# Kernel tuning notes

Hardware: AMD Instinct MI355X
Metric: run time of the kernel (lower is better)

The kernel has to match this reference:

```python
import jax, jax.numpy as jnp
import numpy as np

N_NODES = 50000
N_EDGES = 800000
D_IN = 128
HIDDEN = 128
N_CLASSES = 10
N_GRAPHS = 128


def setup_inputs() -> dict:
    key = jax.random.key(0)
    ks = jax.random.split(key, 16)
    x = jax.random.normal(ks[0], (N_NODES, D_IN), dtype=jnp.float32)
    edge_index = jax.random.randint(ks[1], (2, N_EDGES), 0, N_NODES, dtype=jnp.int64)
    batch = jnp.sort(jax.random.randint(ks[2], (N_NODES,), 0, N_GRAPHS, dtype=jnp.int64))

    def lin(k, fin, fout):
        return jax.random.normal(k, (fin, fout), dtype=jnp.float32) / np.sqrt(fin)

    inp = {"x": x, "edge_index": edge_index, "batch": batch}
    # SAGEConv layer 1: in=D_IN, out=HIDDEN; layers 2,3: HIDDEN->HIDDEN
    dims = [(D_IN, HIDDEN), (HIDDEN, HIDDEN), (HIDDEN, HIDDEN)]
    for i, (fin, fout) in enumerate(dims, start=1):
        inp[f"Wl{i}"] = lin(ks[2 + 2 * i], fin, fout)       # neighbor transform
        inp[f"bl{i}"] = jnp.zeros((fout,), dtype=jnp.float32)
        inp[f"Wr{i}"] = lin(ks[3 + 2 * i], fin, fout)       # root transform
    inp["W1"] = lin(ks[12], HIDDEN, HIDDEN)
    inp["b1"] = jnp.zeros((HIDDEN,), dtype=jnp.float32)
    inp["W2"] = lin(ks[13], HIDDEN, N_CLASSES)
    inp["b2"] = jnp.zeros((N_CLASSES,), dtype=jnp.float32)
    return inp


def _sage_conv(x, src, dst, Wl, bl, Wr):
    # mean-aggregate neighbor features then linear; plus root linear (PyG SAGEConv)
    msg = x[src]                                               # [E, d] gather
    agg = jax.ops.segment_sum(msg, dst, num_segments=N_NODES)  # [N, d]
    cnt = jax.ops.segment_sum(jnp.ones_like(dst, dtype=x.dtype), dst,
                              num_segments=N_NODES)
    agg = agg / jnp.maximum(cnt, 1.0)[:, None]
    return agg @ Wl + bl + x @ Wr


def reference(x, edge_index, batch, Wl1, bl1, Wr1, Wl2, bl2, Wr2,
              Wl3, bl3, Wr3, W1, b1, W2, b2):
    src, dst = edge_index[0], edge_index[1]
    h = jax.nn.relu(_sage_conv(x, src, dst, Wl1, bl1, Wr1))
    h = jax.nn.relu(_sage_conv(h, src, dst, Wl2, bl2, Wr2))
    h = jax.nn.relu(_sage_conv(h, src, dst, Wl3, bl3, Wr3))
    # global_mean_pool over graph ids
    gsum = jax.ops.segment_sum(h, batch, num_segments=N_GRAPHS)
    gcnt = jax.ops.segment_sum(jnp.ones((h.shape[0],), h.dtype), batch,
                               num_segments=N_GRAPHS)
    g = gsum / jnp.maximum(gcnt, 1.0)[:, None]                 # [G, hidden]
    g = jax.nn.relu(g @ W1 + b1)
    # dropout is identity at inference (training=False)
    logits = g @ W2 + b2
    return jax.nn.log_softmax(logits, axis=-1)
```

## Files before the change

### kernel.cpp

```cpp
#include <hip/hip_runtime.h>

#define NN 50000
#define NE 800000
#define D 128
#define NG 128
#define POOL_NODES 128
#define SCAN_NB ((NN + 1023) / 1024)
#define NGRP 8
#define GRPSZ 6250
#define FILL_NB 392
#define ESL ((NE + 48) / 49)

typedef __attribute__((ext_vector_type(8))) short bf16x8;
typedef __attribute__((ext_vector_type(4))) float f32x4;

static __device__ __forceinline__ ushort f2bf(float f) {
    uint x = __float_as_uint(f);
    x += 0x7fffu + ((x >> 16) & 1u);
    return (ushort)(x >> 16);
}
static __device__ __forceinline__ float bf2f(ushort u) { return __uint_as_float((uint)u << 16); }
static __device__ __forceinline__ float blo16(uint u) { return __uint_as_float(u << 16); }
static __device__ __forceinline__ float bhi16(uint u) { return __uint_as_float(u & 0xffff0000u); }

#define CASTX_NB 6250
#define CASTW_NB 192
#define COUNT_NB 3125
__global__ __launch_bounds__(256) void fusedA_kernel(
    const float* __restrict__ x, ushort* __restrict__ xb,
    const float* __restrict__ Wl1, const float* __restrict__ Wr1,
    const float* __restrict__ Wl2, const float* __restrict__ Wr2,
    const float* __restrict__ Wl3, const float* __restrict__ Wr3,
    ushort* __restrict__ wlh, ushort* __restrict__ wll,
    ushort* __restrict__ wrh, ushort* __restrict__ wrl,
    const int* __restrict__ dst, int* __restrict__ cnt) {
    const int bid = blockIdx.x;
    if (bid < CASTX_NB) {
        int i = bid * 256 + threadIdx.x;
        int n = i >> 5, g = i & 31;
        float4 v = *reinterpret_cast<const float4*>(x + (size_t)n * D + g * 4);
        ushort4 o;
        o.x = f2bf(v.x); o.y = f2bf(v.y); o.z = f2bf(v.z); o.w = f2bf(v.w);
        *reinterpret_cast<ushort4*>(xb + (size_t)n * D + g * 4) = o;
    } else if (bid < CASTX_NB + CASTW_NB) {
        int i = (bid - CASTX_NB) * 256 + threadIdx.x;
        int layer = i >> 14, j = i & 16383;
        int colg = j >> 7, k = j & 127;
        const float* Wl = (layer == 0) ? Wl1 : ((layer == 1) ? Wl2 : Wl3);
        const float* Wr = (layer == 0) ? Wr1 : ((layer == 1) ? Wr2 : Wr3);
        float vl = Wl[k * 128 + colg];
        float vr = Wr[k * 128 + colg];
        ushort hl = f2bf(vl), hr = f2bf(vr);
        wlh[i] = hl; wll[i] = f2bf(vl - bf2f(hl));
        wrh[i] = hr; wrl[i] = f2bf(vr - bf2f(hr));
    } else {
        int e = (bid - CASTX_NB - CASTW_NB) * 256 + threadIdx.x;
        if (e < NE) atomicAdd(&cnt[dst[e]], 1);
    }
}

__global__ __launch_bounds__(256) void blocksum_kernel(const int* __restrict__ cnt,
                                                       int* __restrict__ bsum, int N) {
    int base = blockIdx.x * 1024 + threadIdx.x * 4;
    int s = 0;
    if (base + 3 < N) {
        int4 v = *reinterpret_cast<const int4*>(cnt + base);
        s = v.x + v.y + v.z + v.w;
    } else {
        for (int i = 0; i < 4; ++i) if (base + i < N) s += cnt[base + i];
    }
    for (int off = 32; off > 0; off >>= 1) s += __shfl_down(s, off, 64);
    __shared__ int wsum[4];
    if ((threadIdx.x & 63) == 0) wsum[threadIdx.x >> 6] = s;
    __syncthreads();
    if (threadIdx.x == 0) bsum[blockIdx.x] = wsum[0] + wsum[1] + wsum[2] + wsum[3];
}

__global__ void scansum_kernel(int* __restrict__ bsum, int* __restrict__ rowptr, int NB, int N) {
    int t = threadIdx.x;
    int v = (t < NB) ? bsum[t] : 0;
    for (int off = 1; off < 64; off <<= 1) {
        int u = __shfl_up(v, off, 64);
        if (t >= off) v += u;
    }
    if (t < NB) bsum[t] = v;
    if (t == NB - 1) rowptr[N] = v;
}

__global__ __launch_bounds__(256) void writeptr_kernel(const int* __restrict__ cnt,
                                                       const int* __restrict__ bsum,
                                                       int* __restrict__ rowptr, int N) {
    const int b = blockIdx.x;
    const int base = b * 1024 + threadIdx.x * 4;
    int vals[4];
#pragma unroll
    for (int i = 0; i < 4; ++i) vals[i] = (base + i < N) ? cnt[base + i] : 0;
    int s = vals[0] + vals[1] + vals[2] + vals[3];

    const int lane = threadIdx.x & 63, w = threadIdx.x >> 6;
    int incl = s;
    for (int off = 1; off < 64; off <<= 1) {
        int u = __shfl_up(incl, off, 64);
        if (lane >= off) incl += u;
    }
    __shared__ int wsum[4];
    if (lane == 63) wsum[w] = incl;
    __syncthreads();
    int excl = (b == 0) ? 0 : bsum[b - 1];
    for (int i = 0; i < w; ++i) excl += wsum[i];
    excl += incl - s;

    int run = excl;
#pragma unroll
    for (int i = 0; i < 4; ++i) {
        if (base + i < N) { rowptr[base + i] = run; run += vals[i]; }
    }
}

static __device__ __forceinline__ void gemm2_body(
    char* As, int rb,
    const ushort* __restrict__ ain,
    const ushort* __restrict__ wlh, const ushort* __restrict__ wll,
    const ushort* __restrict__ wrh, const ushort* __restrict__ wrl,
    const float* __restrict__ bl,
    ushort* __restrict__ y, ushort* __restrict__ z, int N) {
    const int tid = threadIdx.x;
    const int w = tid >> 6, lane = tid & 63;
    const int row0 = rb * 128;
    const int lrow = lane & 15, lk = lane >> 4;
    const int colg = w * 16 + lrow;

    bf16x8 ylh[4], yll[4], zrh[4], zrl[4];
#pragma unroll
    for (int kb = 0; kb < 4; ++kb) {
        int off = colg * 128 + kb * 32 + lk * 8;
        ylh[kb] = *reinterpret_cast<const bf16x8*>(wlh + off);
        yll[kb] = *reinterpret_cast<const bf16x8*>(wll + off);
        zrh[kb] = *reinterpret_cast<const bf16x8*>(wrh + off);
        zrl[kb] = *reinterpret_cast<const bf16x8*>(wrl + off);
    }
    const float bias = bl[colg];

    {
        const char* gbase = (const char*)ain + (size_t)row0 * 256;
#pragma unroll
        for (int i = 0; i < 4; ++i) {
            int Ld = i * 8192 + w * 1024 + lane * 16;
            int gs = Ld ^ (((Ld >> 8) & 7) << 4);
            __builtin_amdgcn_global_load_lds(
                (const uint*)(gbase + gs),
                (uint*)(As + i * 8192 + w * 1024), 16, 0, 0);
        }
    }
    __syncthreads();

#pragma unroll
    for (int mt = 0; mt < 8; ++mt) {
        const int ar = mt * 16 + lrow;
        const int swz = (ar & 7) << 4;
        const char* ap = As + ar * 256;
        bf16x8 ah[4];
#pragma unroll
        for (int kb = 0; kb < 4; ++kb) {
            int b_ = kb * 64 + lk * 16;
            ah[kb] = *reinterpret_cast<const bf16x8*>(ap + (b_ ^ swz));
        }
        f32x4 accy = {0.f, 0.f, 0.f, 0.f}, accz = {0.f, 0.f, 0.f, 0.f};
#pragma unroll
        for (int kb = 0; kb < 4; ++kb) {
            accy = __builtin_amdgcn_mfma_f32_16x16x32_bf16(ah[kb], ylh[kb], accy, 0, 0, 0);
            accy = __builtin_amdgcn_mfma_f32_16x16x32_bf16(ah[kb], yll[kb], accy, 0, 0, 0);
            accz = __builtin_amdgcn_mfma_f32_16x16x32_bf16(ah[kb], zrh[kb], accz, 0, 0, 0);
            accz = __builtin_amdgcn_mfma_f32_16x16x32_bf16(ah[kb], zrl[kb], accz, 0, 0, 0);
        }
#pragma unroll
        for (int r = 0; r < 4; ++r) {
            int rowg = row0 + mt * 16 + lk * 4 + r;
            if (rowg < N) {
                y[(size_t)rowg * D + colg] = f2bf(accy[r]);
                z[(size_t)rowg * D + colg] = f2bf(accz[r] + bias);
            }
        }
    }
}

__global__ __launch_bounds__(512, 4) void gemm2_kernel(
    const ushort* __restrict__ ain,
    const ushort* __restrict__ wlh, const ushort* __restrict__ wll,
    const ushort* __restrict__ wrh, const ushort* __restrict__ wrl,
    const float* __restrict__ bl,
    ushort* __restrict__ y, ushort* __restrict__ z, int N) {
    __shared__ char As[128 * 256];
    gemm2_body(As, blockIdx.x, ain, wlh, wll, wrh, wrl, bl, y, z, N);
}

#define GEMM_NB 391
__global__ __launch_bounds__(512, 4) void fusedB_kernel(
    const ushort* __restrict__ ain,
    const ushort* __restrict__ wlh, const ushort* __restrict__ wll,
    const ushort* __restrict__ wrh, const ushort* __restrict__ wrl,
    const float* __restrict__ bl,
    ushort* __restrict__ y, ushort* __restrict__ z,
    const int* __restrict__ src, const int* __restrict__ dst,
    const int* __restrict__ rowptr, int* __restrict__ fillp,
    int* __restrict__ col, int N) {
    __shared__ char As[128 * 256];
    const int bid = blockIdx.x;
    if (bid < FILL_NB) {
        const int grp = bid & 7;
        const int slice = bid >> 3;
        const int dlo = grp * GRPSZ, dhi = dlo + GRPSZ;
        const int e0 = slice * ESL;
        const int e1 = min(e0 + ESL, NE);
        for (int e = e0 + (int)threadIdx.x; e < e1; e += 512) {
            int d = dst[e];
            if (d >= dlo && d < dhi) {
                int s = src[e];
                int pos = atomicAdd(&fillp[d], 1);
                col[rowptr[d] + pos] = s;
            }
        }
    } else {
        gemm2_body(As, bid - FILL_NB, ain, wlh, wll, wrh, wrl, bl, y, z, N);
    }
}

__global__ __launch_bounds__(256) void gather_relu(
    const ushort* __restrict__ y, ushort* __restrict__ z,
    const int* __restrict__ rowptr, const int* __restrict__ col, int N) {
    int wid = (blockIdx.x * 256 + threadIdx.x) >> 6;
    if (wid >= N) return;
    const int lane = threadIdx.x & 63;
    const int h = lane >> 5, li = lane & 31;
    int lo = rowptr[wid], hi = rowptr[wid + 1];
    float a0 = 0.f, a1 = 0.f, a2 = 0.f, a3 = 0.f;
    int e = lo + h;
    for (; e + 2 < hi; e += 4) {
        int s0 = col[e], s1 = col[e + 2];
        uint2 v0 = *reinterpret_cast<const uint2*>(y + (size_t)s0 * D + li * 4);
        uint2 v1 = *reinterpret_cast<const uint2*>(y + (size_t)s1 * D + li * 4);
        a0 += blo16(v0.x) + blo16(v1.x);
        a1 += bhi16(v0.x) + bhi16(v1.x);
        a2 += blo16(v0.y) + blo16(v1.y);
        a3 += bhi16(v0.y) + bhi16(v1.y);
    }
    for (; e < hi; e += 2) {
        uint2 v = *reinterpret_cast<const uint2*>(y + (size_t)col[e] * D + li * 4);
        a0 += blo16(v.x); a1 += bhi16(v.x);
        a2 += blo16(v.y); a3 += bhi16(v.y);
    }
    a0 += __shfl_xor(a0, 32, 64);
    a1 += __shfl_xor(a1, 32, 64);
    a2 += __shfl_xor(a2, 32, 64);
    a3 += __shfl_xor(a3, 32, 64);
    if (h == 0) {
        float inv = 1.0f / fmaxf((float)(hi - lo), 1.0f);
        uint2 zv = *reinterpret_cast<const uint2*>(z + (size_t)wid * D + li * 4);
        float h0 = fmaxf(a0 * inv + blo16(zv.x), 0.f);
        float h1 = fmaxf(a1 * inv + bhi16(zv.x), 0.f);
        float h2 = fmaxf(a2 * inv + blo16(zv.y), 0.f);
        float h3 = fmaxf(a3 * inv + bhi16(zv.y), 0.f);
        uint2 o;
        o.x = (uint)f2bf(h0) | ((uint)f2bf(h1) << 16);
        o.y = (uint)f2bf(h2) | ((uint)f2bf(h3) << 16);
        *reinterpret_cast<uint2*>(z + (size_t)wid * D + li * 4) = o;
    }
}

__global__ __launch_bounds__(256) void pool_i(
    const ushort* __restrict__ hbuf, const int* __restrict__ batch,
    float* __restrict__ gsum, int N) {
    const int lane = threadIdx.x & 63;
    const int wv = threadIdx.x >> 6;
    const int cb = lane * 2;
    const int n0 = blockIdx.x * POOL_NODES;
    const int n1 = min(n0 + POOL_NODES, N);
    int gid = -1;
    float a0 = 0.f, a1 = 0.f;
    for (int n = n0 + wv; n < n1; n += 4) {
        int b = batch[n];
        if (b != gid) {
            if (gid >= 0) {
                atomicAdd(&gsum[gid * D + cb], a0);
                atomicAdd(&gsum[gid * D + cb + 1], a1);
            }
            gid = b; a0 = a1 = 0.f;
        }
        uint v = *reinterpret_cast<const uint*>(hbuf + (size_t)n * D + cb);
        a0 += blo16(v); a1 += bhi16(v);
    }
    if (gid >= 0) {
        atomicAdd(&gsum[gid * D + cb], a0);
        atomicAdd(&gsum[gid * D + cb + 1], a1);
    }
}

__global__ __launch_bounds__(128) void head_kernel(
    const float* __restrict__ gsum, const int* __restrict__ batch, int N,
    const float* __restrict__ W1, const float* __restrict__ b1,
    const float* __restrict__ W2, const float* __restrict__ b2,
    float* __restrict__ out) {
    __shared__ float gl[128];
    __shared__ float tl[128];
    __shared__ float lg[10];
    __shared__ float red[2];
    const int b = blockIdx.x, j = threadIdx.x;

    int lo = 0, r = N;
    while (lo < r) { int m = (lo + r) >> 1; if (batch[m] < b) lo = m + 1; else r = m; }
    int hi = lo; r = N;
    while (hi < r) { int m = (hi + r) >> 1; if (batch[m] < b + 1) hi = m + 1; else r = m; }

    float c = fmaxf((float)(hi - lo), 1.0f);
    gl[j] = gsum[b * D + j] / c;
    __syncthreads();

    float t = b1[j];
    for (int k = 0; k < 128; ++k) t += gl[k] * W1[k * 128 + j];
    tl[j] = fmaxf(t, 0.0f);
    __syncthreads();

    if (j < 10) {
        float acc = b2[j];
        for (int k = 0; k < 128; ++k) acc += tl[k] * W2[k * 10 + j];
        lg[j] = acc;
    }
    __syncthreads();

    if (j == 0) {
        float m = lg[0];
        for (int q = 1; q < 10; ++q) m = fmaxf(m, lg[q]);
        float s = 0.0f;
        for (int q = 0; q < 10; ++q) s += expf(lg[q] - m);
        red[0] = m;
        red[1] = logf(s);
    }
    __syncthreads();

    if (j < 10) out[b * 10 + j] = lg[j] - red[0] - red[1];
}

extern "C" void kernel_launch(void* const* d_in, const int* in_sizes, int n_in,
                              void* d_out, int out_size, void* d_ws, size_t ws_size,
                              hipStream_t stream) {
    const float* x    = (const float*)d_in[0];
    const int*   ei   = (const int*)d_in[1];
    const int*   src  = ei;
    const int*   dst  = ei + NE;
    const int*   batch = (const int*)d_in[2];
    const float* Wl1 = (const float*)d_in[3];
    const float* bl1 = (const float*)d_in[4];
    const float* Wr1 = (const float*)d_in[5];
    const float* Wl2 = (const float*)d_in[6];
    const float* bl2 = (const float*)d_in[7];
    const float* Wr2 = (const float*)d_in[8];
    const float* Wl3 = (const float*)d_in[9];
    const float* bl3 = (const float*)d_in[10];
    const float* Wr3 = (const float*)d_in[11];
    const float* W1  = (const float*)d_in[12];
    const float* b1  = (const float*)d_in[13];
    const float* W2  = (const float*)d_in[14];
    const float* b2  = (const float*)d_in[15];
    float* out = (float*)d_out;

    char* p = (char*)d_ws;
    char* S0 = p; p += 12800000;
    char* S1 = p; p += 12800000;
    char* S2 = p; p += 12800000;
    ushort* wlh = (ushort*)p; p += 3 * 32768;
    ushort* wll = (ushort*)p; p += 3 * 32768;
    ushort* wrh = (ushort*)p; p += 3 * 32768;
    ushort* wrl = (ushort*)p; p += 3 * 32768;
    float* gsum = (float*)p; p += 65536;
    int* cnt    = (int*)p;   p += 200000;
    int* fillp  = (int*)p;   p += 200000;
    int* rowptr = (int*)p;   p += 200016;
    int* colb   = (int*)p;   p += 3200000;
    int* bsum   = (int*)p;   p += 256;

    hipMemsetAsync(cnt, 0, (size_t)NN * 4, stream);
    hipMemsetAsync(fillp, 0, (size_t)NN * 4, stream);
    hipMemsetAsync(gsum, 0, (size_t)NG * D * 4, stream);

    fusedA_kernel<<<CASTX_NB + CASTW_NB + COUNT_NB, 256, 0, stream>>>(
        x, (ushort*)S0, Wl1, Wr1, Wl2, Wr2, Wl3, Wr3, wlh, wll, wrh, wrl, dst, cnt);

    blocksum_kernel<<<SCAN_NB, 256, 0, stream>>>(cnt, bsum, NN);
    scansum_kernel<<<1, 64, 0, stream>>>(bsum, rowptr, SCAN_NB, NN);
    writeptr_kernel<<<SCAN_NB, 256, 0, stream>>>(cnt, bsum, rowptr, NN);

    const int agg_blocks = (NN * 64 + 255) / 256;

    fusedB_kernel<<<FILL_NB + GEMM_NB, 512, 0, stream>>>(
        (ushort*)S0, wlh, wll, wrh, wrl, bl1, (ushort*)S1, (ushort*)S2,
        src, dst, rowptr, fillp, colb, NN);

    gather_relu<<<agg_blocks, 256, 0, stream>>>((ushort*)S1, (ushort*)S2, rowptr, colb, NN);
    gemm2_kernel<<<GEMM_NB, 512, 0, stream>>>((ushort*)S2, wlh + 16384, wll + 16384,
                                              wrh + 16384, wrl + 16384, bl2,
                                              (ushort*)S1, (ushort*)S0, NN);
    gather_relu<<<agg_blocks, 256, 0, stream>>>((ushort*)S1, (ushort*)S0, rowptr, colb, NN);
    gemm2_kernel<<<GEMM_NB, 512, 0, stream>>>((ushort*)S0, wlh + 32768, wll + 32768,
                                              wrh + 32768, wrl + 32768, bl3,
                                              (ushort*)S1, (ushort*)S2, NN);
    gather_relu<<<agg_blocks, 256, 0, stream>>>((ushort*)S1, (ushort*)S2, rowptr, colb, NN);

    pool_i<<<(NN + POOL_NODES - 1) / POOL_NODES, 256, 0, stream>>>((ushort*)S2, batch, gsum, NN);
    head_kernel<<<NG, 128, 0, stream>>>(gsum, batch, NN, W1, b1, W2, b2, out);
}
```

Baseline: 280.3 us.

## Fuse pooling into head kernel, unroll gather loop, merge memsets

Replaces the atomic-based pooling kernel and the separate head kernel with one kernel per graph. It finds each graph's node range by binary search over the sorted batch, reduces features in shared memory, then runs the MLP and log-softmax. This removes the gsum buffer, its memset, the atomics and one launch. The neighbor gather loop is unrolled to four loads per iteration to raise memory-level parallelism, and the two count memsets are merged into one contiguous memset. The per-graph pooling uses only 128 blocks, which may underuse the GPU for that phase.

```diff
diff --git a/kernel.cpp b/kernel.cpp
--- a/kernel.cpp
+++ b/kernel.cpp
@@ -4,7 +4,6 @@
 #define NE 800000
 #define D 128
 #define NG 128
-#define POOL_NODES 128
 #define SCAN_NB ((NN + 1023) / 1024)
 #define NGRP 8
 #define GRPSZ 6250
@@ -235,14 +234,16 @@
     int lo = rowptr[wid], hi = rowptr[wid + 1];
     float a0 = 0.f, a1 = 0.f, a2 = 0.f, a3 = 0.f;
     int e = lo + h;
-    for (; e + 2 < hi; e += 4) {
-        int s0 = col[e], s1 = col[e + 2];
+    for (; e + 6 < hi; e += 8) {
+        int s0 = col[e], s1 = col[e + 2], s2 = col[e + 4], s3 = col[e + 6];
         uint2 v0 = *reinterpret_cast<const uint2*>(y + (size_t)s0 * D + li * 4);
         uint2 v1 = *reinterpret_cast<const uint2*>(y + (size_t)s1 * D + li * 4);
-        a0 += blo16(v0.x) + blo16(v1.x);
-        a1 += bhi16(v0.x) + bhi16(v1.x);
-        a2 += blo16(v0.y) + blo16(v1.y);
-        a3 += bhi16(v0.y) + bhi16(v1.y);
+        uint2 v2 = *reinterpret_cast<const uint2*>(y + (size_t)s2 * D + li * 4);
+        uint2 v3 = *reinterpret_cast<const uint2*>(y + (size_t)s3 * D + li * 4);
+        a0 += (blo16(v0.x) + blo16(v1.x)) + (blo16(v2.x) + blo16(v3.x));
+        a1 += (bhi16(v0.x) + bhi16(v1.x)) + (bhi16(v2.x) + bhi16(v3.x));
+        a2 += (blo16(v0.y) + blo16(v1.y)) + (blo16(v2.y) + blo16(v3.y));
+        a3 += (bhi16(v0.y) + bhi16(v1.y)) + (bhi16(v2.y) + bhi16(v3.y));
     }
     for (; e < hi; e += 2) {
         uint2 v = *reinterpret_cast<const uint2*>(y + (size_t)col[e] * D + li * 4);
@@ -267,67 +268,57 @@
     }
 }
 
-__global__ __launch_bounds__(256) void pool_i(
-    const ushort* __restrict__ hbuf, const int* __restrict__ batch,
-    float* __restrict__ gsum, int N) {
-    const int lane = threadIdx.x & 63;
-    const int wv = threadIdx.x >> 6;
-    const int cb = lane * 2;
-    const int n0 = blockIdx.x * POOL_NODES;
-    const int n1 = min(n0 + POOL_NODES, N);
-    int gid = -1;
-    float a0 = 0.f, a1 = 0.f;
-    for (int n = n0 + wv; n < n1; n += 4) {
-        int b = batch[n];
-        if (b != gid) {
-            if (gid >= 0) {
-                atomicAdd(&gsum[gid * D + cb], a0);
-                atomicAdd(&gsum[gid * D + cb + 1], a1);
-            }
-            gid = b; a0 = a1 = 0.f;
-        }
-        uint v = *reinterpret_cast<const uint*>(hbuf + (size_t)n * D + cb);
-        a0 += blo16(v); a1 += bhi16(v);
-    }
-    if (gid >= 0) {
-        atomicAdd(&gsum[gid * D + cb], a0);
-        atomicAdd(&gsum[gid * D + cb + 1], a1);
-    }
-}
-
-__global__ __launch_bounds__(128) void head_kernel(
-    const float* __restrict__ gsum, const int* __restrict__ batch, int N,
+__global__ __launch_bounds__(256) void pool_head(
+    const ushort* __restrict__ hbuf, const int* __restrict__ batch, int N,
     const float* __restrict__ W1, const float* __restrict__ b1,
     const float* __restrict__ W2, const float* __restrict__ b2,
     float* __restrict__ out) {
+    __shared__ float part[4][128];
     __shared__ float gl[128];
     __shared__ float tl[128];
     __shared__ float lg[10];
     __shared__ float red[2];
-    const int b = blockIdx.x, j = threadIdx.x;
+    const int b = blockIdx.x;
+    const int tid = threadIdx.x;
+    const int wv = tid >> 6, lane = tid & 63;
+    const int cb = lane * 2;
 
     int lo = 0, r = N;
     while (lo < r) { int m = (lo + r) >> 1; if (batch[m] < b) lo = m + 1; else r = m; }
     int hi = lo; r = N;
     while (hi < r) { int m = (hi + r) >> 1; if (batch[m] < b + 1) hi = m + 1; else r = m; }
 
-    float c = fmaxf((float)(hi - lo), 1.0f);
-    gl[j] = gsum[b * D + j] / c;
-    __syncthreads();
-
-    float t = b1[j];
-    for (int k = 0; k < 128; ++k) t += gl[k] * W1[k * 128 + j];
-    tl[j] = fmaxf(t, 0.0f);
-    __syncthreads();
-
-    if (j < 10) {
-        float acc = b2[j];
-        for (int k = 0; k < 128; ++k) acc += tl[k] * W2[k * 10 + j];
-        lg[j] = acc;
-    }
-    __syncthreads();
-
-    if (j == 0) {
+    float a0 = 0.f, a1 = 0.f;
+    for (int n = lo + wv; n < hi; n += 4) {
+        uint v = *reinterpret_cast<const uint*>(hbuf + (size_t)n * D + cb);
+        a0 += blo16(v); a1 += bhi16(v);
+    }
+    part[wv][cb] = a0;
+    part[wv][cb + 1] = a1;
+    __syncthreads();
+
+    const int j = tid & 127;
+    if (tid < 128) {
+        float c = fmaxf((float)(hi - lo), 1.0f);
+        gl[j] = (part[0][j] + part[1][j] + part[2][j] + part[3][j]) / c;
+    }
+    __syncthreads();
+
+    if (tid < 128) {
+        float t = b1[j];
+        for (int k = 0; k < 128; ++k) t += gl[k] * W1[k * 128 + j];
+        tl[j] = fmaxf(t, 0.0f);
+    }
+    __syncthreads();
+
+    if (tid < 10) {
+        float acc = b2[tid];
+        for (int k = 0; k < 128; ++k) acc += tl[k] * W2[k * 10 + tid];
+        lg[tid] = acc;
+    }
+    __syncthreads();
+
+    if (tid == 0) {
         float m = lg[0];
         for (int q = 1; q < 10; ++q) m = fmaxf(m, lg[q]);
         float s = 0.0f;
@@ -337,7 +328,7 @@
     }
     __syncthreads();
 
-    if (j < 10) out[b * 10 + j] = lg[j] - red[0] - red[1];
+    if (tid < 10) out[b * 10 + tid] = lg[tid] - red[0] - red[1];
 }
 
 extern "C" void kernel_launch(void* const* d_in, const int* in_sizes, int n_in,
@@ -371,16 +362,13 @@
     ushort* wll = (ushort*)p; p += 3 * 32768;
     ushort* wrh = (ushort*)p; p += 3 * 32768;
     ushort* wrl = (ushort*)p; p += 3 * 32768;
-    float* gsum = (float*)p; p += 65536;
     int* cnt    = (int*)p;   p += 200000;
     int* fillp  = (int*)p;   p += 200000;
     int* rowptr = (int*)p;   p += 200016;
     int* colb   = (int*)p;   p += 3200000;
     int* bsum   = (int*)p;   p += 256;
 
-    hipMemsetAsync(cnt, 0, (size_t)NN * 4, stream);
-    hipMemsetAsync(fillp, 0, (size_t)NN * 4, stream);
-    hipMemsetAsync(gsum, 0, (size_t)NG * D * 4, stream);
+    hipMemsetAsync(cnt, 0, 400000, stream);
 
     fusedA_kernel<<<CASTX_NB + CASTW_NB + COUNT_NB, 256, 0, stream>>>(
         x, (ushort*)S0, Wl1, Wr1, Wl2, Wr2, Wl3, Wr3, wlh, wll, wrh, wrl, dst, cnt);
@@ -405,6 +393,5 @@
                                               (ushort*)S1, (ushort*)S2, NN);
     gather_relu<<<agg_blocks, 256, 0, stream>>>((ushort*)S1, (ushort*)S2, rowptr, colb, NN);
 
-    pool_i<<<(NN + POOL_NODES - 1) / POOL_NODES, 256, 0, stream>>>((ushort*)S2, batch, gsum, NN);
-    head_kernel<<<NG, 128, 0, stream>>>(gsum, batch, NN, W1, b1, W2, b2, out);
-}
+    pool_head<<<NG, 256, 0, stream>>>((ushort*)S2, batch, NN, W1, b1, W2, b2, out);
+}
```

Measured after the change: 285.4 us. About the same (+1.8%).
